# Kernel tuning notes

Measured on AMD Instinct MI355X. Metric: run time of the kernel, lower is better.

## Reference

```python
import jax, jax.numpy as jnp
import numpy as np

B, S, H = 2, 2048, 2048
NH, NKV, HD = 32, 4, 128
THETA = 1e6
EPS = 1e-6


def setup_inputs() -> dict:
    key = jax.random.key(0)
    ks = jax.random.split(key, 6)
    scale = 0.02
    hidden_states = jax.random.normal(ks[0], (B, S, H), jnp.float32)
    attention_mask = jnp.broadcast_to(jnp.tril(jnp.ones((S, S), bool))[None, None], (B, 1, S, S))
    position_ids = jnp.broadcast_to(jnp.arange(S, dtype=jnp.int32), (B, S))
    Wq = jax.random.normal(ks[1], (H, NH * HD), jnp.float32) * scale
    Wk = jax.random.normal(ks[2], (H, NKV * HD), jnp.float32) * scale
    Wv = jax.random.normal(ks[3], (H, NKV * HD), jnp.float32) * scale
    Wo = jax.random.normal(ks[4], (NH * HD, H), jnp.float32) * scale
    q_norm_w = jnp.ones((HD,), jnp.float32)
    k_norm_w = jnp.ones((HD,), jnp.float32)
    return dict(hidden_states=hidden_states, attention_mask=attention_mask,
                position_ids=position_ids, Wq=Wq, Wk=Wk, Wv=Wv, Wo=Wo,
                q_norm_w=q_norm_w, k_norm_w=k_norm_w)


def _rms_norm(x, w):
    # per-head RMSNorm over last dim (head_dim)
    var = jnp.mean(x * x, axis=-1, keepdims=True)
    return x * jax.lax.rsqrt(var + EPS) * w


def _rotate_half(x):
    x1, x2 = jnp.split(x, 2, axis=-1)
    return jnp.concatenate([-x2, x1], axis=-1)


def _rope(position_ids):
    inv_freq = 1.0 / (THETA ** (jnp.arange(0, HD, 2, dtype=jnp.float32) / HD))  # [HD/2]
    freqs = position_ids.astype(jnp.float32)[..., None] * inv_freq  # [B,S,HD/2]
    emb = jnp.concatenate([freqs, freqs], axis=-1)  # [B,S,HD]
    return jnp.cos(emb), jnp.sin(emb)


def reference(hidden_states, attention_mask, position_ids, Wq, Wk, Wv, Wo, q_norm_w, k_norm_w):
    cos, sin = _rope(position_ids)               # [B,S,HD]
    cos = cos[:, :, None, :]                     # [B,S,1,HD] broadcast over heads
    sin = sin[:, :, None, :]

    q = (hidden_states @ Wq).reshape(B, S, NH, HD)
    k = (hidden_states @ Wk).reshape(B, S, NKV, HD)
    v = (hidden_states @ Wv).reshape(B, S, NKV, HD)

    q = _rms_norm(q, q_norm_w)
    k = _rms_norm(k, k_norm_w)

    q = q * cos + _rotate_half(q) * sin
    k = k * cos + _rotate_half(k) * sin

    # GQA: repeat each kv head NH//NKV times (matches HF repeat_kv ordering)
    k = jnp.repeat(k, NH // NKV, axis=2)         # [B,S,NH,HD]
    v = jnp.repeat(v, NH // NKV, axis=2)

    q = q.transpose(0, 2, 1, 3)                  # [B,NH,S,HD]
    k = k.transpose(0, 2, 1, 3)
    v = v.transpose(0, 2, 1, 3)

    scores = jnp.einsum('bhqd,bhkd->bhqk', q, k) * (HD ** -0.5)
    scores = jnp.where(attention_mask, scores, jnp.finfo(scores.dtype).min)
    attn = jax.nn.softmax(scores, axis=-1)
    ctx = jnp.einsum('bhqk,bhkd->bhqd', attn, v)  # [B,NH,S,HD]
    ctx = ctx.transpose(0, 2, 1, 3).reshape(B, S, NH * HD)
    return ctx @ Wo                               # [B,S,H]
```

## Files before the change

kernel.cpp:

```cpp
#include <hip/hip_runtime.h>
#include <stdint.h>
#include <stddef.h>

typedef unsigned short ushort_t;
typedef unsigned int uint32;

typedef _Float16 half8 __attribute__((ext_vector_type(8)));
typedef _Float16 half4 __attribute__((ext_vector_type(4)));
typedef float f32x4 __attribute__((ext_vector_type(4)));

#define NLINV (-0.2158673600755816f)
#define INV2PI 0.15915494309189535f
#define TWOPI 6.283185307179586f
#define FPITCH 40

#define GLDS(gptr, lptr)                                                                   \
  __builtin_amdgcn_global_load_lds((const __attribute__((address_space(1))) unsigned int*)(gptr), \
                                   (__attribute__((address_space(3))) unsigned int*)(lptr), \
                                   16, 0, 0)

static __device__ __forceinline__ float bf_lo(uint32 u) { union { uint32 u; float f; } v; v.u = u << 16; return v.f; }
static __device__ __forceinline__ float bf_hi(uint32 u) { union { uint32 u; float f; } v; v.u = u & 0xffff0000u; return v.f; }
static __device__ __forceinline__ ushort_t f2bf(float f) {
  union { float f; uint32 u; } v; v.f = f;
  return (ushort_t)((v.u + 0x7fffu + ((v.u >> 16) & 1u)) >> 16);
}
static __device__ __forceinline__ half8 cvt8(uint4 u) {
  half8 h;
  h[0] = (_Float16)bf_lo(u.x); h[1] = (_Float16)bf_hi(u.x);
  h[2] = (_Float16)bf_lo(u.y); h[3] = (_Float16)bf_hi(u.y);
  h[4] = (_Float16)bf_lo(u.z); h[5] = (_Float16)bf_hi(u.z);
  h[6] = (_Float16)bf_lo(u.w); h[7] = (_Float16)bf_hi(u.w);
  return h;
}
static __device__ __forceinline__ half8 load8h(const void* p, int mode, size_t eidx) {
  if (mode == 2) return ((const half8*)p)[eidx >> 3];
  if (mode == 1) {
    const float4* q = (const float4*)p + (eidx >> 2);
    const float4 a = q[0], b = q[1];
    half8 h;
    h[0] = (_Float16)a.x; h[1] = (_Float16)a.y; h[2] = (_Float16)a.z; h[3] = (_Float16)a.w;
    h[4] = (_Float16)b.x; h[5] = (_Float16)b.y; h[6] = (_Float16)b.z; h[7] = (_Float16)b.w;
    return h;
  }
  return cvt8(((const uint4*)p)[eidx >> 3]);
}
static __device__ __forceinline__ float wval(const void* w, int is_f32, int i) {
  if (is_f32) return ((const float*)w)[i];
  union { uint32 u; float f; } v; v.u = ((uint32)((const ushort_t*)w)[i]) << 16; return v.f;
}
static __device__ __forceinline__ int probe_f32(const void* p) {
  const uint32 u = ((const uint32*)p)[threadIdx.x & 63];
  const int e = (u >> 7) & 0xff;
  return __popcll(__ballot(e >= 110 && e <= 135)) < 32 ? 1 : 0;
}

__global__ __launch_bounds__(256) void probe_fill(uint32* out, uint32 pat, int nwords) {
  for (int i = blockIdx.x * 256 + threadIdx.x; i < nwords; i += gridDim.x * 256) out[i] = pat;
}

__global__ __launch_bounds__(256) void convert_hs(const void* __restrict__ hs,
                                                  _Float16* __restrict__ hsF, int n8) {
  const int f = probe_f32(hs);
  for (int i = blockIdx.x * 256 + threadIdx.x; i < n8; i += gridDim.x * 256)
    ((half8*)hsF)[i] = load8h(hs, f, (size_t)i << 3);
}

__global__ __launch_bounds__(256) void transpose_w(const void* __restrict__ W, int K, int N,
                                                   _Float16* __restrict__ Wt) {
  __shared__ __align__(16) _Float16 T[64][72];
  const int fw = probe_f32(W);
  const int n0 = blockIdx.x * 64, k0 = blockIdx.y * 64;
  const int tid = threadIdx.x;
  const int r = tid >> 2, cc = (tid & 3) * 16;
  const size_t src = (size_t)(k0 + r) * N + n0 + cc;
  const half8 v0 = load8h(W, fw, src);
  const half8 v1 = load8h(W, fw, src + 8);
  *(half8*)&T[r][cc] = v0;
  *(half8*)&T[r][cc + 8] = v1;
  __syncthreads();
  half8 o0, o1;
#pragma unroll
  for (int j = 0; j < 8; ++j) { o0[j] = T[cc + j][r]; o1[j] = T[cc + 8 + j][r]; }
  _Float16* dst = Wt + (size_t)(n0 + r) * K + k0 + cc;
  *(half8*)dst = o0;
  *(half8*)(dst + 8) = o1;
}


__global__ __launch_bounds__(256) void gemm2_rope(const _Float16* __restrict__ Af, int lda,
                                                  int arow0, const _Float16* __restrict__ Bt,
                                                  int ldb, _Float16* __restrict__ C, int ldc,
                                                  int K, const void* __restrict__ w) {
  __shared__ __align__(16) _Float16 As[128 * 32];
  __shared__ __align__(16) _Float16 Bs[128 * 32];
  __shared__ float Ct[64 * 128];
  const int fw = probe_f32(w);
  const int tid = threadIdx.x;
  const int wave = tid >> 6, lane = tid & 63;
  const int m0 = blockIdx.y * 128, n0 = blockIdx.x * 128;
  const int wm = (wave >> 1) * 64, wn = (wave & 1) * 64;
  const int fr = lane & 15, quad = lane >> 4;
  const int r0 = wave * 32 + (lane >> 2);
  const int r1 = r0 + 16;
  const int cs0 = ((lane & 3) ^ ((r0 >> 1) & 3)) << 3;
  const int cs1 = ((lane & 3) ^ ((r1 >> 1) & 3)) << 3;
  const _Float16* Ar0 = Af + (size_t)(arow0 + m0 + r0) * lda + cs0;
  const _Float16* Ar1 = Af + (size_t)(arow0 + m0 + r1) * lda + cs1;
  const _Float16* Br0 = Bt + (size_t)(n0 + r0) * ldb + cs0;
  const _Float16* Br1 = Bt + (size_t)(n0 + r1) * ldb + cs1;
  _Float16* lA0 = &As[(wave * 32) * 32];
  _Float16* lA1 = &As[(wave * 32 + 16) * 32];
  _Float16* lB0 = &Bs[(wave * 32) * 32];
  _Float16* lB1 = &Bs[(wave * 32 + 16) * 32];
  f32x4 acc[4][4] = {};
  for (int k0 = 0; k0 < K; k0 += 32) {
    __syncthreads();
    GLDS(Ar0 + k0, lA0);
    GLDS(Ar1 + k0, lA1);
    GLDS(Br0 + k0, lB0);
    GLDS(Br1 + k0, lB1);
    __syncthreads();
    half8 a[4], b[4];
#pragma unroll
    for (int t = 0; t < 4; ++t) {
      const int row = wm + t * 16 + fr;
      a[t] = *(const half8*)&As[row * 32 + ((quad ^ ((row >> 1) & 3)) << 3)];
    }
#pragma unroll
    for (int t = 0; t < 4; ++t) {
      const int row = wn + t * 16 + fr;
      b[t] = *(const half8*)&Bs[row * 32 + ((quad ^ ((row >> 1) & 3)) << 3)];
    }
#pragma unroll
    for (int mt = 0; mt < 4; ++mt)
#pragma unroll
      for (int nt = 0; nt < 4; ++nt)
        acc[mt][nt] = __builtin_amdgcn_mfma_f32_16x16x32_f16(a[mt], b[nt], acc[mt][nt], 0, 0, 0);
  }
  __syncthreads();
#pragma unroll
  for (int hf = 0; hf < 2; ++hf) {
    if ((wave >> 1) == hf) {
#pragma unroll
      for (int mt = 0; mt < 4; ++mt)
#pragma unroll
        for (int nt = 0; nt < 4; ++nt)
#pragma unroll
          for (int r = 0; r < 4; ++r)
            Ct[(mt * 16 + quad * 4 + r) * 128 + wn + nt * 16 + fr] = acc[mt][nt][r];
    }
    __syncthreads();
    const int row = tid >> 2, sub = tid & 3;
    float ss = 0.f;
#pragma unroll
    for (int j = 0; j < 32; ++j) {
      const float v = Ct[row * 128 + sub * 32 + j];
      ss += v * v;
    }
    ss += __shfl_xor(ss, 1);
    ss += __shfl_xor(ss, 2);
    const float rinv = rsqrtf(ss * (1.0f / 128.0f) + 1e-6f);
    const int grow = m0 + hf * 64 + row;
    const int s = (arow0 + grow) & 2047;
    uint32 obuf[16];
#pragma unroll
    for (int j = 0; j < 32; j += 2) {
      float o2[2];
#pragma unroll
      for (int e = 0; e < 2; ++e) {
        const int c = sub * 32 + j + e;
        const float x = Ct[row * 128 + c];
        const float p = Ct[row * 128 + (c ^ 64)];
        const float xn = x * rinv * wval(w, fw, c);
        const float pn = p * rinv * wval(w, fw, c ^ 64);
        const float rot = (c < 64) ? -pn : pn;
        const float fq = __expf((float)(c & 63) * NLINV);
        float rev = (float)s * fq * INV2PI;
        rev -= rintf(rev);
        float sn, cs;
        __sincosf(rev * TWOPI, &sn, &cs);
        o2[e] = xn * cs + rot * sn;
      }
      union { _Float16 h[2]; uint32 u; } pk;
      pk.h[0] = (_Float16)o2[0]; pk.h[1] = (_Float16)o2[1];
      obuf[j >> 1] = pk.u;
    }
    uint32* dst = (uint32*)(C + (size_t)grow * ldc + n0 + sub * 32);
#pragma unroll
    for (int j2 = 0; j2 < 16; ++j2) dst[j2] = obuf[j2];
    __syncthreads();
  }
}

__global__ __launch_bounds__(256) void gemm2_plain(const _Float16* __restrict__ Af, int lda,
                                                   int arow0, const _Float16* __restrict__ Bt,
                                                   int ldb, char* __restrict__ obase,
                                                   size_t oeoff, int ldc, int omode, int K,
                                                   const void* __restrict__ pES) {
  __shared__ __align__(16) _Float16 As[128 * 32];
  __shared__ __align__(16) _Float16 Bs[128 * 32];
  const int fes = probe_f32(pES);
  const int tid = threadIdx.x;
  const int wave = tid >> 6, lane = tid & 63;
  const int m0 = blockIdx.y * 128, n0 = blockIdx.x * 128;
  const int wm = (wave >> 1) * 64, wn = (wave & 1) * 64;
  const int fr = lane & 15, quad = lane >> 4;
  const int r0 = wave * 32 + (lane >> 2);
  const int r1 = r0 + 16;
  const int cs0 = ((lane & 3) ^ ((r0 >> 1) & 3)) << 3;
  const int cs1 = ((lane & 3) ^ ((r1 >> 1) & 3)) << 3;
  const _Float16* Ar0 = Af + (size_t)(arow0 + m0 + r0) * lda + cs0;
  const _Float16* Ar1 = Af + (size_t)(arow0 + m0 + r1) * lda + cs1;
  const _Float16* Br0 = Bt + (size_t)(n0 + r0) * ldb + cs0;
  const _Float16* Br1 = Bt + (size_t)(n0 + r1) * ldb + cs1;
  _Float16* lA0 = &As[(wave * 32) * 32];
  _Float16* lA1 = &As[(wave * 32 + 16) * 32];
  _Float16* lB0 = &Bs[(wave * 32) * 32];
  _Float16* lB1 = &Bs[(wave * 32 + 16) * 32];
  f32x4 acc[4][4] = {};
  for (int k0 = 0; k0 < K; k0 += 32) {
    __syncthreads();
    GLDS(Ar0 + k0, lA0);
    GLDS(Ar1 + k0, lA1);
    GLDS(Br0 + k0, lB0);
    GLDS(Br1 + k0, lB1);
    __syncthreads();
    half8 a[4], b[4];
#pragma unroll
    for (int t = 0; t < 4; ++t) {
      const int row = wm + t * 16 + fr;
      a[t] = *(const half8*)&As[row * 32 + ((quad ^ ((row >> 1) & 3)) << 3)];
    }
#pragma unroll
    for (int t = 0; t < 4; ++t) {
      const int row = wn + t * 16 + fr;
      b[t] = *(const half8*)&Bs[row * 32 + ((quad ^ ((row >> 1) & 3)) << 3)];
    }
#pragma unroll
    for (int mt = 0; mt < 4; ++mt)
#pragma unroll
      for (int nt = 0; nt < 4; ++nt)
        acc[mt][nt] = __builtin_amdgcn_mfma_f32_16x16x32_f16(a[mt], b[nt], acc[mt][nt], 0, 0, 0);
  }
  if (omode == 2) {
#pragma unroll
    for (int mt = 0; mt < 4; ++mt)
#pragma unroll
      for (int nt = 0; nt < 4; ++nt) {
        half4 pk;
#pragma unroll
        for (int r = 0; r < 4; ++r) pk[r] = (_Float16)acc[mt][nt][r];
        *(half4*)((_Float16*)obase + (size_t)(n0 + wn + nt * 16 + fr) * ldc +
                  m0 + wm + mt * 16 + quad * 4) = pk;
      }
    return;
  }
#pragma unroll
  for (int mt = 0; mt < 4; ++mt)
#pragma unroll
    for (int nt = 0; nt < 4; ++nt)
#pragma unroll
      for (int r = 0; r < 4; ++r) {
        const size_t idx = (size_t)(m0 + wm + mt * 16 + quad * 4 + r) * ldc + n0 + wn + nt * 16 + fr;
        const float v = acc[mt][nt][r];
        if (fes) ((float*)obase)[oeoff + idx] = v;
        else ((ushort_t*)obase)[oeoff + idx] = f2bf(v);
      }
}

__global__ __launch_bounds__(256) void gemm_rope_fast(const void* __restrict__ Araw, int lda,
                                                      int arow0, const _Float16* __restrict__ Bt,
                                                      int ldb, char* __restrict__ obase,
                                                      size_t oeoff, int ldc, int K,
                                                      const void* __restrict__ w) {
  __shared__ __align__(16) _Float16 As[128 * FPITCH];
  __shared__ __align__(16) _Float16 Bs[128 * FPITCH];
  __shared__ float Ct[64 * 128];
  const int fa = probe_f32(Araw);
  const int fw = probe_f32(w);
  _Float16* Cv = (_Float16*)(obase + oeoff * (fa ? 4u : 2u));
  const int tid = threadIdx.x;
  const int wave = tid >> 6, lane = tid & 63;
  const int m0 = blockIdx.y * 128, n0 = blockIdx.x * 128;
  const int wm = (wave >> 1) * 64, wn = (wave & 1) * 64;
  const int fr = lane & 15, quad = lane >> 4;
  const int sr = tid >> 1, sc = (tid & 1) * 16;
  f32x4 acc[4][4] = {};
  for (int k0 = 0; k0 < K; k0 += 32) {
    const size_t aidx = (size_t)(arow0 + m0 + sr) * lda + k0 + sc;
    const half8 av0 = load8h(Araw, fa, aidx);
    const half8 av1 = load8h(Araw, fa, aidx + 8);
    const _Float16* bp = Bt + (size_t)(n0 + sr) * ldb + k0 + sc;
    const half8 bv0 = *(const half8*)bp;
    const half8 bv1 = *(const half8*)(bp + 8);
    __syncthreads();
    *(half8*)&As[sr * FPITCH + sc] = av0;
    *(half8*)&As[sr * FPITCH + sc + 8] = av1;
    *(half8*)&Bs[sr * FPITCH + sc] = bv0;
    *(half8*)&Bs[sr * FPITCH + sc + 8] = bv1;
    __syncthreads();
    half8 a[4], b[4];
#pragma unroll
    for (int t = 0; t < 4; ++t)
      a[t] = *(const half8*)&As[(wm + t * 16 + fr) * FPITCH + quad * 8];
#pragma unroll
    for (int t = 0; t < 4; ++t)
      b[t] = *(const half8*)&Bs[(wn + t * 16 + fr) * FPITCH + quad * 8];
#pragma unroll
    for (int mt = 0; mt < 4; ++mt)
#pragma unroll
      for (int nt = 0; nt < 4; ++nt)
        acc[mt][nt] = __builtin_amdgcn_mfma_f32_16x16x32_f16(a[mt], b[nt], acc[mt][nt], 0, 0, 0);
  }
  __syncthreads();
#pragma unroll
  for (int hf = 0; hf < 2; ++hf) {
    if ((wave >> 1) == hf) {
#pragma unroll
      for (int mt = 0; mt < 4; ++mt)
#pragma unroll
        for (int nt = 0; nt < 4; ++nt)
#pragma unroll
          for (int r = 0; r < 4; ++r)
            Ct[(mt * 16 + quad * 4 + r) * 128 + wn + nt * 16 + fr] = acc[mt][nt][r];
    }
    __syncthreads();
    const int row = tid >> 2, sub = tid & 3;
    float ss = 0.f;
#pragma unroll
    for (int j = 0; j < 32; ++j) {
      const float v = Ct[row * 128 + sub * 32 + j];
      ss += v * v;
    }
    ss += __shfl_xor(ss, 1);
    ss += __shfl_xor(ss, 2);
    const float rinv = rsqrtf(ss * (1.0f / 128.0f) + 1e-6f);
    const int grow = m0 + hf * 64 + row;
    const int s = (arow0 + grow) & 2047;
    uint32 obuf[16];
#pragma unroll
    for (int j = 0; j < 32; j += 2) {
      float o2[2];
#pragma unroll
      for (int e = 0; e < 2; ++e) {
        const int c = sub * 32 + j + e;
        const float x = Ct[row * 128 + c];
        const float p = Ct[row * 128 + (c ^ 64)];
        const float xn = x * rinv * wval(w, fw, c);
        const float pn = p * rinv * wval(w, fw, c ^ 64);
        const float rot = (c < 64) ? -pn : pn;
        const float fq = __expf((float)(c & 63) * NLINV);
        float rev = (float)s * fq * INV2PI;
        rev -= rintf(rev);
        float sn, cs;
        __sincosf(rev * TWOPI, &sn, &cs);
        o2[e] = xn * cs + rot * sn;
      }
      union { _Float16 h[2]; uint32 u; } pk;
      pk.h[0] = (_Float16)o2[0]; pk.h[1] = (_Float16)o2[1];
      obuf[j >> 1] = pk.u;
    }
    uint32* dst = (uint32*)(Cv + (size_t)grow * ldc + n0 + sub * 32);
#pragma unroll
    for (int j2 = 0; j2 < 16; ++j2) dst[j2] = obuf[j2];
    __syncthreads();
  }
}

__global__ __launch_bounds__(256) void gemm_plain_fast(const char* __restrict__ abase, size_t aeoff,
                                                       int lda, int amode, int arow0,
                                                       const _Float16* __restrict__ Bt, int ldb,
                                                       char* __restrict__ obase, size_t oeoff,
                                                       int ldc, int omode, int K,
                                                       const void* __restrict__ pES) {
  __shared__ __align__(16) _Float16 As[128 * FPITCH];
  __shared__ __align__(16) _Float16 Bs[128 * FPITCH];
  const int fes = probe_f32(pES);
  const uint32 es = fes ? 4u : 2u;
  const void* A = abase + aeoff * es;
  const int fa = (amode == 2) ? 2 : probe_f32(abase);
  const int tid = threadIdx.x;
  const int wave = tid >> 6, lane = tid & 63;
  const int m0 = blockIdx.y * 128, n0 = blockIdx.x * 128;
  const int wm = (wave >> 1) * 64, wn = (wave & 1) * 64;
  const int fr = lane & 15, quad = lane >> 4;
  const int sr = tid >> 1, sc = (tid & 1) * 16;
  f32x4 acc[4][4] = {};
  for (int k0 = 0; k0 < K; k0 += 32) {
    const size_t aidx = (size_t)(arow0 + m0 + sr) * lda + k0 + sc;
    const half8 av0 = load8h(A, fa, aidx);
    const half8 av1 = load8h(A, fa, aidx + 8);
    const _Float16* bp = Bt + (size_t)(n0 + sr) * ldb + k0 + sc;
    const half8 bv0 = *(const half8*)bp;
    const half8 bv1 = *(const half8*)(bp + 8);
    __syncthreads();
    *(half8*)&As[sr * FPITCH + sc] = av0;
    *(half8*)&As[sr * FPITCH + sc + 8] = av1;
    *(half8*)&Bs[sr * FPITCH + sc] = bv0;
    *(half8*)&Bs[sr * FPITCH + sc + 8] = bv1;
    __syncthreads();
    half8 a[4], b[4];
#pragma unroll
    for (int t = 0; t < 4; ++t)
      a[t] = *(const half8*)&As[(wm + t * 16 + fr) * FPITCH + quad * 8];
#pragma unroll
    for (int t = 0; t < 4; ++t)
      b[t] = *(const half8*)&Bs[(wn + t * 16 + fr) * FPITCH + quad * 8];
#pragma unroll
    for (int mt = 0; mt < 4; ++mt)
#pragma unroll
      for (int nt = 0; nt < 4; ++nt)
        acc[mt][nt] = __builtin_amdgcn_mfma_f32_16x16x32_f16(a[mt], b[nt], acc[mt][nt], 0, 0, 0);
  }
  if (omode == 2) {
#pragma unroll
    for (int mt = 0; mt < 4; ++mt)
#pragma unroll
      for (int nt = 0; nt < 4; ++nt) {
        half4 pk;
#pragma unroll
        for (int r = 0; r < 4; ++r) pk[r] = (_Float16)acc[mt][nt][r];
        *(half4*)((_Float16*)obase + (size_t)(n0 + wn + nt * 16 + fr) * ldc +
                  m0 + wm + mt * 16 + quad * 4) = pk;
      }
    return;
  }
#pragma unroll
  for (int mt = 0; mt < 4; ++mt)
#pragma unroll
    for (int nt = 0; nt < 4; ++nt)
#pragma unroll
      for (int r = 0; r < 4; ++r) {
        const size_t idx = (size_t)(m0 + wm + mt * 16 + quad * 4 + r) * ldc + n0 + wn + nt * 16 + fr;
        const float v = acc[mt][nt][r];
        if (omode == 1) ((_Float16*)obase)[idx] = (_Float16)v;
        else if (fes) ((float*)obase)[oeoff + idx] = v;
        else ((ushort_t*)obase)[oeoff + idx] = f2bf(v);
      }
}

#define LOADKV(J0)                                                                             \
  {                                                                                            \
    _Pragma("unroll") for (int ii = 0; ii < 4; ++ii) {                                         \
      const int i = tid + ii * 256;                                                            \
      const int r = i >> 4, c = i & 15;                                                        \
      kreg[ii] = *(const half8*)(K + (size_t)((J0) + r) * 512 + kv * 128 + ((c ^ (r & 7)) << 3)); \
      const int d = i >> 3, c2 = i & 7;                                                        \
      vreg[ii] = *(const half8*)(V + (size_t)(kv * 128 + d) * 2048 + (J0) + ((c2 ^ (d & 7)) << 3)); \
    }                                                                                          \
  }

__global__ __launch_bounds__(256, 2) void attn_fwd(char* __restrict__ qbase, size_t qeoff,
                                                   const _Float16* __restrict__ Kb,
                                                   const _Float16* __restrict__ Vb, int c0,
                                                   const void* __restrict__ pES) {
  __shared__ __align__(16) _Float16 Ks[64 * 128];
  __shared__ __align__(16) _Float16 Vt[128 * 64];
  __shared__ __align__(16) _Float16 Ps[4 * 16 * 64];
  const uint32 es = probe_f32(pES) ? 4u : 2u;
  const int z = blockIdx.z;
  _Float16* Qbuf = (_Float16*)(qbase + qeoff * es) + (size_t)z * (2048u * 4096u);
  const _Float16* K = Kb + (size_t)z * (2048u * 512u);
  const _Float16* V = Vb + (size_t)z * (512u * 2048u);
  const int tid = threadIdx.x;
  const int wave = tid >> 6, lane = tid & 63;
  const int fr = lane & 15, quad = lane >> 4;
  const int h = blockIdx.y, kv = h >> 3;
  const int nbx = gridDim.x;
  const int bx = blockIdx.x;
  const int pbx = (bx & 1) ? (nbx - 1 - (bx >> 1)) : (bx >> 1);
  const int qb0 = pbx * 64;
  const int qg = c0 + qb0;
  const int qrow0 = qb0 + wave * 16;
  _Float16* Pw = &Ps[wave * 1024];
  half8 qa[4];
#pragma unroll
  for (int kt = 0; kt < 4; ++kt)
    qa[kt] = *(const half8*)(Qbuf + (size_t)(qrow0 + fr) * 4096 + h * 128 + kt * 32 + quad * 8);
  f32x4 Oa[8];
#pragma unroll
  for (int dt = 0; dt < 8; ++dt) Oa[dt] = (f32x4)0.f;
  float mr[4], lr[4];
#pragma unroll
  for (int r = 0; r < 4; ++r) { mr[r] = -1e30f; lr[r] = 0.f; }
  const int ntiles = qg / 64 + 1;
  half8 kreg[4], vreg[4];
  LOADKV(0);
  for (int t = 0; t < ntiles; ++t) {
    __syncthreads();
#pragma unroll
    for (int ii = 0; ii < 4; ++ii) {
      *(half8*)&Ks[(tid + ii * 256) * 8] = kreg[ii];
      *(half8*)&Vt[(tid + ii * 256) * 8] = vreg[ii];
    }
    __syncthreads();
    if (t + 1 < ntiles) LOADKV((t + 1) * 64);
    f32x4 s[4];
#pragma unroll
    for (int nt = 0; nt < 4; ++nt) s[nt] = (f32x4)0.f;
#pragma unroll
    for (int kt = 0; kt < 4; ++kt)
#pragma unroll
      for (int nt = 0; nt < 4; ++nt) {
        const int row = nt * 16 + fr;
        const int boff = ((row << 8) + ((kt * 32 + quad * 8) << 1)) ^ ((row & 7) << 4);
        const half8 kb = *(const half8*)((const char*)Ks + boff);
        s[nt] = __builtin_amdgcn_mfma_f32_16x16x32_f16(qa[kt], kb, s[nt], 0, 0, 0);
      }
    const float SC = 0.08838834764831845f;
    const int j0 = t * 64;
    if (t == ntiles - 1) {
#pragma unroll
      for (int nt = 0; nt < 4; ++nt)
#pragma unroll
        for (int r = 0; r < 4; ++r) {
          const int kpos = j0 + nt * 16 + fr;
          const int qpos = qg + wave * 16 + quad * 4 + r;
          s[nt][r] = (kpos > qpos) ? -1e30f : s[nt][r] * SC;
        }
    } else {
#pragma unroll
      for (int nt = 0; nt < 4; ++nt)
#pragma unroll
        for (int r = 0; r < 4; ++r) s[nt][r] *= SC;
    }
    float al[4];
#pragma unroll
    for (int r = 0; r < 4; ++r) {
      float mx = fmaxf(fmaxf(s[0][r], s[1][r]), fmaxf(s[2][r], s[3][r]));
      mx = fmaxf(mx, __shfl_xor(mx, 1));
      mx = fmaxf(mx, __shfl_xor(mx, 2));
      mx = fmaxf(mx, __shfl_xor(mx, 4));
      mx = fmaxf(mx, __shfl_xor(mx, 8));
      const float mn = fmaxf(mr[r], mx);
      al[r] = __expf(mr[r] - mn);
      mr[r] = mn;
    }
    float rs[4] = {0.f, 0.f, 0.f, 0.f};
#pragma unroll
    for (int nt = 0; nt < 4; ++nt)
#pragma unroll
      for (int r = 0; r < 4; ++r) {
        const float p = __expf(s[nt][r] - mr[r]);
        rs[r] += p;
        const int q = quad * 4 + r;
        const int boff = (((q << 7) + ((nt * 16 + fr) << 1)) ^ ((q & 7) << 4));
        *(_Float16*)((char*)Pw + boff) = (_Float16)p;
      }
#pragma unroll
    for (int r = 0; r < 4; ++r) {
      rs[r] += __shfl_xor(rs[r], 1);
      rs[r] += __shfl_xor(rs[r], 2);
      rs[r] += __shfl_xor(rs[r], 4);
      rs[r] += __shfl_xor(rs[r], 8);
      lr[r] = lr[r] * al[r] + rs[r];
    }
#pragma unroll
    for (int dt = 0; dt < 8; ++dt)
#pragma unroll
      for (int r = 0; r < 4; ++r) Oa[dt][r] *= al[r];
    half8 pa[2];
#pragma unroll
    for (int kt = 0; kt < 2; ++kt) {
      const int boff = (((fr << 7) + ((kt * 32 + quad * 8) << 1)) ^ ((fr & 7) << 4));
      pa[kt] = *(const half8*)((const char*)Pw + boff);
    }
#pragma unroll
    for (int dt = 0; dt < 8; ++dt)
#pragma unroll
      for (int kt = 0; kt < 2; ++kt) {
        const int d = dt * 16 + fr;
        const int boff = (((d << 7) + ((kt * 32 + quad * 8) << 1)) ^ ((d & 7) << 4));
        const half8 vb = *(const half8*)((const char*)Vt + boff);
        Oa[dt] = __builtin_amdgcn_mfma_f32_16x16x32_f16(pa[kt], vb, Oa[dt], 0, 0, 0);
      }
  }
#pragma unroll
  for (int r = 0; r < 4; ++r) {
    const float linv = 1.0f / lr[r];
    _Float16* orow = Qbuf + (size_t)(qrow0 + quad * 4 + r) * 4096 + h * 128;
#pragma unroll
    for (int dt = 0; dt < 8; ++dt) orow[dt * 16 + fr] = (_Float16)(Oa[dt][r] * linv);
  }
}

extern "C" void kernel_launch(void* const* d_in, const int* in_sizes, int n_in,
                              void* d_out, int out_size, void* d_ws, size_t ws_size,
                              hipStream_t stream) {
  (void)in_sizes; (void)n_in; (void)out_size;
  const void* hs = d_in[0];
  const void* Wq = d_in[3];
  const void* Wk = d_in[4];
  const void* Wv = d_in[5];
  const void* Wo = d_in[6];
  const void* qw = d_in[7];
  const void* kw = d_in[8];
  char* dout = (char*)d_out;
  const size_t MB = 1048576;

  probe_fill<<<2048, 256, 0, stream>>>((uint32*)d_out, 0x42C842C8u, 4194304);
  if (ws_size < 40 * MB) {
    probe_fill<<<2048, 256, 0, stream>>>((uint32*)d_out, 0x43484348u, 4194304);
    return;
  }

  if (ws_size >= 92 * MB) {
    _Float16* Kb2 = (_Float16*)d_ws;
    _Float16* Vb2 = (_Float16*)((char*)d_ws + 4 * MB);
    _Float16* WqT = (_Float16*)((char*)d_ws + 8 * MB);
    _Float16* WoT = (_Float16*)((char*)d_ws + 24 * MB);
    _Float16* WkT = (_Float16*)((char*)d_ws + 40 * MB);
    _Float16* WvT = (_Float16*)((char*)d_ws + 42 * MB);
    _Float16* Qw2 = (_Float16*)((char*)d_ws + 44 * MB);
    _Float16* hsF = (_Float16*)((char*)d_ws + 76 * MB);
    transpose_w<<<dim3(64, 32), 256, 0, stream>>>(Wq, 2048, 4096, WqT);
    transpose_w<<<dim3(8, 32), 256, 0, stream>>>(Wk, 2048, 512, WkT);
    transpose_w<<<dim3(8, 32), 256, 0, stream>>>(Wv, 2048, 512, WvT);
    transpose_w<<<dim3(32, 64), 256, 0, stream>>>(Wo, 4096, 2048, WoT);
    convert_hs<<<2048, 256, 0, stream>>>(hs, hsF, 1048576);
    for (int b = 0; b < 2; ++b) {
      gemm2_rope<<<dim3(4, 16), 256, 0, stream>>>(hsF, 2048, b * 2048, WkT, 2048,
                                                  Kb2 + (size_t)b * 1048576, 512, 2048, kw);
      gemm2_plain<<<dim3(4, 16), 256, 0, stream>>>(hsF, 2048, b * 2048, WvT, 2048,
                                                   (char*)(Vb2 + (size_t)b * 1048576), 0, 2048,
                                                   2, 2048, hs);
      gemm2_rope<<<dim3(32, 16), 256, 0, stream>>>(hsF, 2048, b * 2048, WqT, 2048,
                                                   Qw2 + (size_t)b * 8388608, 4096, 2048, qw);
    }
    attn_fwd<<<dim3(32, 32, 2), 256, 0, stream>>>((char*)Qw2, 0, Kb2, Vb2, 0, hs);
    for (int b = 0; b < 2; ++b)
      gemm2_plain<<<dim3(16, 16), 256, 0, stream>>>(Qw2 + (size_t)b * 8388608, 4096, 0,
                                                    WoT, 4096, dout, (size_t)b * 4194304, 2048,
                                                    0, 4096, hs);
    return;
  }

  _Float16* Kbuf = (_Float16*)d_ws;
  _Float16* Vbuf = (_Float16*)((char*)d_ws + 2 * MB);
  _Float16* WqT = (_Float16*)((char*)d_ws + 4 * MB);
  _Float16* WoT = (_Float16*)((char*)d_ws + 20 * MB);
  _Float16* WkT = (_Float16*)((char*)d_ws + 36 * MB);
  _Float16* WvT = (_Float16*)((char*)d_ws + 38 * MB);
  const size_t QOFF = 4194304;

  transpose_w<<<dim3(64, 32), 256, 0, stream>>>(Wq, 2048, 4096, WqT);
  transpose_w<<<dim3(8, 32), 256, 0, stream>>>(Wk, 2048, 512, WkT);
  transpose_w<<<dim3(8, 32), 256, 0, stream>>>(Wv, 2048, 512, WvT);
  transpose_w<<<dim3(32, 64), 256, 0, stream>>>(Wo, 4096, 2048, WoT);

  if (ws_size >= 72 * MB) {
    char* Qw = (char*)d_ws + 40 * MB;
    _Float16* hsF = (_Float16*)((char*)d_ws + 56 * MB);
    convert_hs<<<2048, 256, 0, stream>>>(hs, hsF, 1048576);
    for (int b = 0; b < 2; ++b) {
      gemm2_rope<<<dim3(4, 16), 256, 0, stream>>>(hsF, 2048, b * 2048, WkT, 2048,
                                                  Kbuf, 512, 2048, kw);
      gemm2_plain<<<dim3(4, 16), 256, 0, stream>>>(hsF, 2048, b * 2048, WvT, 2048,
                                                   (char*)Vbuf, 0, 2048, 2, 2048, hs);
      gemm2_rope<<<dim3(32, 16), 256, 0, stream>>>(hsF, 2048, b * 2048, WqT, 2048,
                                                   (_Float16*)Qw, 4096, 2048, qw);
      attn_fwd<<<dim3(32, 32), 256, 0, stream>>>(Qw, 0, Kbuf, Vbuf, 0, hs);
      gemm2_plain<<<dim3(16, 16), 256, 0, stream>>>((const _Float16*)Qw, 4096, 0, WoT, 4096,
                                                    dout, (size_t)b * 4194304, 2048, 0, 4096, hs);
    }
    return;
  }

  if (ws_size >= 56 * MB) {
    char* Qw = (char*)d_ws + 40 * MB;
    for (int b = 0; b < 2; ++b) {
      gemm_rope_fast<<<dim3(4, 16), 256, 0, stream>>>(hs, 2048, b * 2048, WkT, 2048,
                                                      (char*)Kbuf, 0, 512, 2048, kw);
      gemm_plain_fast<<<dim3(4, 16), 256, 0, stream>>>((const char*)hs, 0, 2048, 0, b * 2048,
                                                       WvT, 2048, (char*)Vbuf, 0, 2048, 2,
                                                       2048, hs);
      gemm_rope_fast<<<dim3(32, 16), 256, 0, stream>>>(hs, 2048, b * 2048, WqT, 2048,
                                                       Qw, 0, 4096, 2048, qw);
      attn_fwd<<<dim3(32, 32), 256, 0, stream>>>(Qw, 0, Kbuf, Vbuf, 0, hs);
      gemm_plain_fast<<<dim3(16, 16), 256, 0, stream>>>((const char*)Qw, 0, 4096, 2, 0,
                                                        WoT, 4096, dout,
                                                        (size_t)b * 4194304, 2048, 0, 4096, hs);
    }
    return;
  }

  for (int b = 0; b < 2; ++b) {
    gemm_rope_fast<<<dim3(4, 16), 256, 0, stream>>>(hs, 2048, b * 2048, WkT, 2048,
                                                    (char*)Kbuf, 0, 512, 2048, kw);
    gemm_plain_fast<<<dim3(4, 16), 256, 0, stream>>>((const char*)hs, 0, 2048, 0, b * 2048,
                                                     WvT, 2048, (char*)Vbuf, 0, 2048, 2,
                                                     2048, hs);
    if (b == 0) {
      for (int c0 = 0; c0 < 2048; c0 += 1024) {
        gemm_rope_fast<<<dim3(32, 8), 256, 0, stream>>>(hs, 2048, c0, WqT, 2048,
                                                        dout, QOFF, 4096, 2048, qw);
        attn_fwd<<<dim3(16, 32), 256, 0, stream>>>(dout, QOFF, Kbuf, Vbuf, c0, hs);
        gemm_plain_fast<<<dim3(16, 8), 256, 0, stream>>>((const char*)dout, QOFF, 4096, 2, 0,
                                                         WoT, 4096, dout, (size_t)c0 * 2048,
                                                         2048, 0, 4096, hs);
      }
    } else {
      const int cs[8][2] = {{1536, 512}, {1024, 512}, {768, 256}, {512, 256},
                            {384, 128}, {256, 128}, {128, 128}, {0, 128}};
      for (int i = 0; i < 8; ++i) {
        const int c0 = cs[i][0], CH = cs[i][1];
        char* qb = (c0 >= 256) ? dout : ((char*)d_ws + 262144);
        const size_t qoff = (c0 >= 256) ? QOFF : 0;
        gemm_rope_fast<<<dim3(32, CH / 128), 256, 0, stream>>>(hs, 2048, 2048 + c0, WqT, 2048,
                                                               qb, qoff, 4096, 2048, qw);
        attn_fwd<<<dim3(CH / 64, 32), 256, 0, stream>>>(qb, qoff, Kbuf, Vbuf, c0, hs);
        gemm_plain_fast<<<dim3(16, CH / 128), 256, 0, stream>>>((const char*)qb, qoff, 4096, 2,
                                                                0, WoT, 4096, dout,
                                                                (size_t)(2048 + c0) * 2048,
                                                                2048, 0, 4096, hs);
      }
    }
  }
}
```

Baseline: 1.128 ms.

## Lazy softmax rescaling, deferred row-sum reduction, and batched projection GEMMs

The attention kernel now rescales the running max and output accumulator only when a row's new max exceeds the old one by more than a threshold, checked wave-uniformly. It keeps per-lane partial row sums and does the cross-lane shuffle reduction once at the end instead of every tile. In the large-workspace path, the per-batch K/V/Q and output GEMM launches are merged into single launches over both batches, with V stored interleaved using a leading dimension of 4096. This cuts per-tile exp/shuffle/multiply work and launch count, but the threshold lets unnormalized probabilities grow up to e^8 before being stored as fp16.

```diff
diff --git a/kernel.cpp b/kernel.cpp
--- a/kernel.cpp
+++ b/kernel.cpp
@@ -447,14 +447,14 @@
       const int r = i >> 4, c = i & 15;                                                        \
       kreg[ii] = *(const half8*)(K + (size_t)((J0) + r) * 512 + kv * 128 + ((c ^ (r & 7)) << 3)); \
       const int d = i >> 3, c2 = i & 7;                                                        \
-      vreg[ii] = *(const half8*)(V + (size_t)(kv * 128 + d) * 2048 + (J0) + ((c2 ^ (d & 7)) << 3)); \
+      vreg[ii] = *(const half8*)(V + (size_t)(kv * 128 + d) * ldv + (J0) + ((c2 ^ (d & 7)) << 3)); \
     }                                                                                          \
   }
 
 __global__ __launch_bounds__(256, 2) void attn_fwd(char* __restrict__ qbase, size_t qeoff,
                                                    const _Float16* __restrict__ Kb,
-                                                   const _Float16* __restrict__ Vb, int c0,
-                                                   const void* __restrict__ pES) {
+                                                   const _Float16* __restrict__ Vb, int ldv,
+                                                   int c0, const void* __restrict__ pES) {
   __shared__ __align__(16) _Float16 Ks[64 * 128];
   __shared__ __align__(16) _Float16 Vt[128 * 64];
   __shared__ __align__(16) _Float16 Ps[4 * 16 * 64];
@@ -462,7 +462,7 @@
   const int z = blockIdx.z;
   _Float16* Qbuf = (_Float16*)(qbase + qeoff * es) + (size_t)z * (2048u * 4096u);
   const _Float16* K = Kb + (size_t)z * (2048u * 512u);
-  const _Float16* V = Vb + (size_t)z * (512u * 2048u);
+  const _Float16* V = Vb + (size_t)z * 2048u;
   const int tid = threadIdx.x;
   const int wave = tid >> 6, lane = tid & 63;
   const int fr = lane & 15, quad = lane >> 4;
@@ -481,9 +481,9 @@
   f32x4 Oa[8];
 #pragma unroll
   for (int dt = 0; dt < 8; ++dt) Oa[dt] = (f32x4)0.f;
-  float mr[4], lr[4];
-#pragma unroll
-  for (int r = 0; r < 4; ++r) { mr[r] = -1e30f; lr[r] = 0.f; }
+  float mr[4], lp[4];
+#pragma unroll
+  for (int r = 0; r < 4; ++r) { mr[r] = -1e30f; lp[r] = 0.f; }
   const int ntiles = qg / 64 + 1;
   half8 kreg[4], vreg[4];
   LOADKV(0);
@@ -525,7 +525,7 @@
 #pragma unroll
         for (int r = 0; r < 4; ++r) s[nt][r] *= SC;
     }
-    float al[4];
+    float mx4[4];
 #pragma unroll
     for (int r = 0; r < 4; ++r) {
       float mx = fmaxf(fmaxf(s[0][r], s[1][r]), fmaxf(s[2][r], s[3][r]));
@@ -533,33 +533,31 @@
       mx = fmaxf(mx, __shfl_xor(mx, 2));
       mx = fmaxf(mx, __shfl_xor(mx, 4));
       mx = fmaxf(mx, __shfl_xor(mx, 8));
-      const float mn = fmaxf(mr[r], mx);
-      al[r] = __expf(mr[r] - mn);
-      mr[r] = mn;
-    }
-    float rs[4] = {0.f, 0.f, 0.f, 0.f};
+      mx4[r] = mx;
+    }
+    const int okl = (mx4[0] <= mr[0] + 8.f) && (mx4[1] <= mr[1] + 8.f) &&
+                    (mx4[2] <= mr[2] + 8.f) && (mx4[3] <= mr[3] + 8.f);
+    if (!__all(okl)) {
+#pragma unroll
+      for (int r = 0; r < 4; ++r) {
+        const float mn = fmaxf(mr[r], mx4[r]);
+        const float al = __expf(mr[r] - mn);
+        mr[r] = mn;
+        lp[r] *= al;
+#pragma unroll
+        for (int dt = 0; dt < 8; ++dt) Oa[dt][r] *= al;
+      }
+    }
 #pragma unroll
     for (int nt = 0; nt < 4; ++nt)
 #pragma unroll
       for (int r = 0; r < 4; ++r) {
         const float p = __expf(s[nt][r] - mr[r]);
-        rs[r] += p;
+        lp[r] += p;
         const int q = quad * 4 + r;
         const int boff = (((q << 7) + ((nt * 16 + fr) << 1)) ^ ((q & 7) << 4));
         *(_Float16*)((char*)Pw + boff) = (_Float16)p;
       }
-#pragma unroll
-    for (int r = 0; r < 4; ++r) {
-      rs[r] += __shfl_xor(rs[r], 1);
-      rs[r] += __shfl_xor(rs[r], 2);
-      rs[r] += __shfl_xor(rs[r], 4);
-      rs[r] += __shfl_xor(rs[r], 8);
-      lr[r] = lr[r] * al[r] + rs[r];
-    }
-#pragma unroll
-    for (int dt = 0; dt < 8; ++dt)
-#pragma unroll
-      for (int r = 0; r < 4; ++r) Oa[dt][r] *= al[r];
     half8 pa[2];
 #pragma unroll
     for (int kt = 0; kt < 2; ++kt) {
@@ -578,7 +576,14 @@
   }
 #pragma unroll
   for (int r = 0; r < 4; ++r) {
-    const float linv = 1.0f / lr[r];
+    lp[r] += __shfl_xor(lp[r], 1);
+    lp[r] += __shfl_xor(lp[r], 2);
+    lp[r] += __shfl_xor(lp[r], 4);
+    lp[r] += __shfl_xor(lp[r], 8);
+  }
+#pragma unroll
+  for (int r = 0; r < 4; ++r) {
+    const float linv = 1.0f / lp[r];
     _Float16* orow = Qbuf + (size_t)(qrow0 + quad * 4 + r) * 4096 + h * 128;
 #pragma unroll
     for (int dt = 0; dt < 8; ++dt) orow[dt * 16 + fr] = (_Float16)(Oa[dt][r] * linv);
@@ -619,20 +624,13 @@
     transpose_w<<<dim3(8, 32), 256, 0, stream>>>(Wv, 2048, 512, WvT);
     transpose_w<<<dim3(32, 64), 256, 0, stream>>>(Wo, 4096, 2048, WoT);
     convert_hs<<<2048, 256, 0, stream>>>(hs, hsF, 1048576);
-    for (int b = 0; b < 2; ++b) {
-      gemm2_rope<<<dim3(4, 16), 256, 0, stream>>>(hsF, 2048, b * 2048, WkT, 2048,
-                                                  Kb2 + (size_t)b * 1048576, 512, 2048, kw);
-      gemm2_plain<<<dim3(4, 16), 256, 0, stream>>>(hsF, 2048, b * 2048, WvT, 2048,
-                                                   (char*)(Vb2 + (size_t)b * 1048576), 0, 2048,
-                                                   2, 2048, hs);
-      gemm2_rope<<<dim3(32, 16), 256, 0, stream>>>(hsF, 2048, b * 2048, WqT, 2048,
-                                                   Qw2 + (size_t)b * 8388608, 4096, 2048, qw);
-    }
-    attn_fwd<<<dim3(32, 32, 2), 256, 0, stream>>>((char*)Qw2, 0, Kb2, Vb2, 0, hs);
-    for (int b = 0; b < 2; ++b)
-      gemm2_plain<<<dim3(16, 16), 256, 0, stream>>>(Qw2 + (size_t)b * 8388608, 4096, 0,
-                                                    WoT, 4096, dout, (size_t)b * 4194304, 2048,
-                                                    0, 4096, hs);
+    gemm2_rope<<<dim3(4, 32), 256, 0, stream>>>(hsF, 2048, 0, WkT, 2048, Kb2, 512, 2048, kw);
+    gemm2_plain<<<dim3(4, 32), 256, 0, stream>>>(hsF, 2048, 0, WvT, 2048, (char*)Vb2, 0, 4096,
+                                                 2, 2048, hs);
+    gemm2_rope<<<dim3(32, 32), 256, 0, stream>>>(hsF, 2048, 0, WqT, 2048, Qw2, 4096, 2048, qw);
+    attn_fwd<<<dim3(32, 32, 2), 256, 0, stream>>>((char*)Qw2, 0, Kb2, Vb2, 4096, 0, hs);
+    gemm2_plain<<<dim3(16, 32), 256, 0, stream>>>(Qw2, 4096, 0, WoT, 4096, dout, 0, 2048,
+                                                  0, 4096, hs);
     return;
   }
 
@@ -660,7 +658,7 @@
                                                    (char*)Vbuf, 0, 2048, 2, 2048, hs);
       gemm2_rope<<<dim3(32, 16), 256, 0, stream>>>(hsF, 2048, b * 2048, WqT, 2048,
                                                    (_Float16*)Qw, 4096, 2048, qw);
-      attn_fwd<<<dim3(32, 32), 256, 0, stream>>>(Qw, 0, Kbuf, Vbuf, 0, hs);
+      attn_fwd<<<dim3(32, 32), 256, 0, stream>>>(Qw, 0, Kbuf, Vbuf, 2048, 0, hs);
       gemm2_plain<<<dim3(16, 16), 256, 0, stream>>>((const _Float16*)Qw, 4096, 0, WoT, 4096,
                                                     dout, (size_t)b * 4194304, 2048, 0, 4096, hs);
     }
@@ -677,7 +675,7 @@
                                                        2048, hs);
       gemm_rope_fast<<<dim3(32, 16), 256, 0, stream>>>(hs, 2048, b * 2048, WqT, 2048,
                                                        Qw, 0, 4096, 2048, qw);
-      attn_fwd<<<dim3(32, 32), 256, 0, stream>>>(Qw, 0, Kbuf, Vbuf, 0, hs);
+      attn_fwd<<<dim3(32, 32), 256, 0, stream>>>(Qw, 0, Kbuf, Vbuf, 2048, 0, hs);
       gemm_plain_fast<<<dim3(16, 16), 256, 0, stream>>>((const char*)Qw, 0, 4096, 2, 0,
                                                         WoT, 4096, dout,
                                                         (size_t)b * 4194304, 2048, 0, 4096, hs);
@@ -695,7 +693,7 @@
       for (int c0 = 0; c0 < 2048; c0 += 1024) {
         gemm_rope_fast<<<dim3(32, 8), 256, 0, stream>>>(hs, 2048, c0, WqT, 2048,
                                                         dout, QOFF, 4096, 2048, qw);
-        attn_fwd<<<dim3(16, 32), 256, 0, stream>>>(dout, QOFF, Kbuf, Vbuf, c0, hs);
+        attn_fwd<<<dim3(16, 32), 256, 0, stream>>>(dout, QOFF, Kbuf, Vbuf, 2048, c0, hs);
         gemm_plain_fast<<<dim3(16, 8), 256, 0, stream>>>((const char*)dout, QOFF, 4096, 2, 0,
                                                          WoT, 4096, dout, (size_t)c0 * 2048,
                                                          2048, 0, 4096, hs);
@@ -709,7 +707,7 @@
         const size_t qoff = (c0 >= 256) ? QOFF : 0;
         gemm_rope_fast<<<dim3(32, CH / 128), 256, 0, stream>>>(hs, 2048, 2048 + c0, WqT, 2048,
                                                                qb, qoff, 4096, 2048, qw);
-        attn_fwd<<<dim3(CH / 64, 32), 256, 0, stream>>>(qb, qoff, Kbuf, Vbuf, c0, hs);
+        attn_fwd<<<dim3(CH / 64, 32), 256, 0, stream>>>(qb, qoff, Kbuf, Vbuf, 2048, c0, hs);
         gemm_plain_fast<<<dim3(16, CH / 128), 256, 0, stream>>>((const char*)qb, qoff, 4096, 2,
                                                                 0, WoT, 4096, dout,
                                                                 (size_t)(2048 + c0) * 2048,
```

New measurement: 928.7 us. -17.6%, faster.
